# Optimization experiments

Hardware: AMD Instinct MI355X
Metric: run time of the kernel (lower is better)

## Reference

```python
import jax, jax.numpy as jnp
import numpy as np

SCALE = 1.0 / (64 ** 0.5)  # 1/sqrt(dim_key)

def setup_inputs() -> dict:
    key = jax.random.key(0)
    ks = jax.random.split(key, 8)
    B, S, D, H, dk = 4, 2048, 1024, 16, 64
    s = 0.02
    return {
        "values": jax.random.normal(ks[0], (B, S, D), jnp.float32),
        "queries": jax.random.normal(ks[1], (B, S, D), jnp.float32),
        "keys": jax.random.normal(ks[2], (B, S, D), jnp.float32),
        "Wq": jax.random.normal(ks[3], (H, D, dk), jnp.float32) * s,
        "bq": jnp.zeros((H, dk), jnp.float32),
        "Wk": jax.random.normal(ks[4], (H, D, dk), jnp.float32) * s,
        "bk": jnp.zeros((H, dk), jnp.float32),
        "Wv": jax.random.normal(ks[5], (H, D, dk), jnp.float32) * s,
        "bv": jnp.zeros((H, dk), jnp.float32),
        "Wo": jax.random.normal(ks[6], (D, D), jnp.float32) * s,
        "bo": jnp.zeros((D,), jnp.float32),
    }

def reference(values, queries, keys, Wq, bq, Wk, bk, Wv, bv, Wo, bo):
    # Per-head projections, batched across heads: [B,S,D] x [H,D,dk] -> [B,H,S,dk]
    q = jnp.einsum('bsd,hdk->bhsk', queries, Wq) + bq[None, :, None, :]
    k = jnp.einsum('bsd,hdk->bhsk', keys, Wk) + bk[None, :, None, :]
    v = jnp.einsum('bsd,hdk->bhsk', values, Wv) + bv[None, :, None, :]
    # Scaled dot-product scores [B,H,S,S]
    scores = jnp.einsum('bhqk,bhsk->bhqs', q, k) * SCALE
    S = scores.shape[-1]
    causal = jnp.tril(jnp.ones((S, S), bool))
    scores = jnp.where(causal, scores, jnp.float32(-1e19))
    attn = jax.nn.softmax(scores, axis=-1)
    ctx = jnp.einsum('bhqs,bhsk->bhqk', attn, v)  # [B,H,S,dk]
    # Concat heads along last axis (head-major, matching tf.concat order)
    B, H, Sq, dk = ctx.shape
    ctx = jnp.transpose(ctx, (0, 2, 1, 3)).reshape(B, Sq, H * dk)
    return ctx @ Wo + bo
```

## Files before the change

kernel.cpp:

```cpp
#include <hip/hip_runtime.h>
#include <hip/hip_bf16.h>
#include <cstdint>

#define B_ 4
#define H_ 16
#define S_ 2048
#define D_ 1024
#define DK 64
#define QSCALE 0.18033688f

typedef float f32x4 __attribute__((ext_vector_type(4)));
typedef short bf8 __attribute__((ext_vector_type(8)));
typedef unsigned short u16;

__device__ __forceinline__ u16 f2bf(float x){
  union { float f; uint32_t u; } c; c.f = x;
  uint32_t u = c.u;
  uint32_t r = (u + 0x7FFFu + ((u >> 16) & 1u)) >> 16;
  return (u16)r;
}

__device__ __forceinline__ uint32_t pk2bf(float a, float b){
  __hip_bfloat162 t = __float22bfloat162_rn(make_float2(a, b));
  uint32_t r; __builtin_memcpy(&r, &t, 4); return r;
}

__device__ __forceinline__ void gl16(const void* g, void* l){
  __builtin_amdgcn_global_load_lds(
      (const __attribute__((address_space(1))) void*)g,
      (__attribute__((address_space(3))) void*)l, 16, 0, 0);
}

__global__ __launch_bounds__(256) void cvt_in(
    const float* __restrict__ q, const float* __restrict__ k,
    const float* __restrict__ v, u16* __restrict__ o)
{
  const size_t N8 = (size_t)1 << 20;
  const size_t tot = 3 * N8;
  const size_t step = (size_t)gridDim.x * 256;
  for (size_t g0 = (size_t)blockIdx.x*256 + threadIdx.x; g0 < tot; g0 += step){
    int t = (int)(g0 >> 20);
    size_t r = g0 & (N8 - 1);
    const float* src = (t==0 ? q : (t==1 ? k : v));
    const float4* s4 = reinterpret_cast<const float4*>(src + r*8);
    float4 a = s4[0], b = s4[1];
    uint4 w;
    w.x = pk2bf(a.x,a.y); w.y = pk2bf(a.z,a.w);
    w.z = pk2bf(b.x,b.y); w.w = pk2bf(b.z,b.w);
    *reinterpret_cast<uint4*>(o + ((size_t)t << 23) + r*8) = w;
  }
}

__global__ __launch_bounds__(256) void wtrans3(
    const float* __restrict__ Wq, const float* __restrict__ Wk,
    const float* __restrict__ Wv, u16* __restrict__ oq,
    u16* __restrict__ ok, u16* __restrict__ ov)
{
  __shared__ u16 T[64*72];
  const int tid = threadIdx.x;
  const int z = blockIdx.z, t = z >> 4, hh = z & 15;
  const float* src = (t==0 ? Wq : t==1 ? Wk : Wv) + (size_t)hh * (D_*DK);
  u16* dst = (t==0 ? oq : t==1 ? ok : ov) + (size_t)hh * (DK*D_);
  const int r0 = blockIdx.y*64;
  #pragma unroll
  for (int p=0;p<4;++p){
    int r  = p*16 + (tid>>4);
    int c4 = (tid&15)*4;
    float4 v = *reinterpret_cast<const float4*>(&src[(size_t)(r0+r)*DK + c4]);
    uint2 w; w.x = pk2bf(v.x, v.y); w.y = pk2bf(v.z, v.w);
    *reinterpret_cast<uint2*>(&T[r*72 + c4]) = w;
  }
  __syncthreads();
  const int c = tid>>2, rg = (tid&3)*16;
  u16 tmp[16];
  #pragma unroll
  for (int i=0;i<16;++i) tmp[i] = T[(rg+i)*72 + c];
  *reinterpret_cast<bf8*>(&dst[(size_t)c*D_ + r0 + rg])     = *reinterpret_cast<bf8*>(&tmp[0]);
  *reinterpret_cast<bf8*>(&dst[(size_t)c*D_ + r0 + rg + 8]) = *reinterpret_cast<bf8*>(&tmp[8]);
}

__global__ __launch_bounds__(256) void wtrans(
    const float* __restrict__ in, u16* __restrict__ out, int R, int C)
{
  __shared__ u16 T[64*72];
  const int tid = threadIdx.x;
  const int r0 = blockIdx.y*64, c0 = blockIdx.x*64;
  #pragma unroll
  for (int p=0;p<4;++p){
    int r  = p*16 + (tid>>4);
    int c4 = (tid&15)*4;
    float4 v = *reinterpret_cast<const float4*>(&in[(size_t)(r0+r)*C + c0 + c4]);
    uint2 w; w.x = pk2bf(v.x, v.y); w.y = pk2bf(v.z, v.w);
    *reinterpret_cast<uint2*>(&T[r*72 + c4]) = w;
  }
  __syncthreads();
  const int c = tid>>2, rg = (tid&3)*16;
  u16 tmp[16];
  #pragma unroll
  for (int i=0;i<16;++i) tmp[i] = T[(rg+i)*72 + c];
  *reinterpret_cast<bf8*>(&out[(size_t)(c0+c)*R + r0 + rg])     = *reinterpret_cast<bf8*>(&tmp[0]);
  *reinterpret_cast<bf8*>(&out[(size_t)(c0+c)*R + r0 + rg + 8]) = *reinterpret_cast<bf8*>(&tmp[8]);
}

__global__ __launch_bounds__(256) void gemm_qkv(
    const u16* __restrict__ Ab,
    const u16* __restrict__ Bq, const u16* __restrict__ Bk,
    const u16* __restrict__ Bv,
    const float* __restrict__ bq, const float* __restrict__ bk,
    const float* __restrict__ bv,
    u16* __restrict__ oq, u16* __restrict__ ok, u16* __restrict__ ov)
{
  __shared__ u16 As[128*64];
  __shared__ u16 Bs[128*64];
  const int tid = threadIdx.x;
  const int wid = tid>>6, lane = tid&63, g = lane>>4, l15 = lane&15;
  const int z = blockIdx.x >> 9, bid = blockIdx.x & 511;
  const u16* A     = Ab + ((size_t)z << 23);
  const u16*   Bt  = (z==0 ? Bq : z==1 ? Bk : Bv);
  const float* bias= (z==0 ? bq : z==1 ? bk : bv);
  u16* Out         = (z==0 ? oq : z==1 ? ok : ov);
  const float osc  = (z==0 ? QSCALE : 1.0f);
  const int xcd = bid & 7, i = bid >> 3;
  const int cb = i & 7, rb = xcd*8 + (i>>3);
  const int row0 = rb*128, col0 = cb*128;
  const int wr = wid>>1, wc = wid&1;

  f32x4 acc[4][4];
  #pragma unroll
  for (int m=0;m<4;++m)
    #pragma unroll
    for (int n=0;n<4;++n) acc[m][n] = (f32x4){0.f,0.f,0.f,0.f};

  for (int k0 = 0; k0 < D_; k0 += 64) {
    #pragma unroll
    for (int p=0;p<4;++p){
      int r0l = wid*32 + p*8;
      int row = r0l + (lane>>3);
      int ch = (lane&7) ^ (row&7);
      gl16(A  + (size_t)(row0+row)*D_ + k0 + ch*8, &As[r0l*64]);
      gl16(Bt + (size_t)(col0+row)*D_ + k0 + ch*8, &Bs[r0l*64]);
    }
    __syncthreads();

    bf8 af[4][2], bfm[4][2];
    #pragma unroll
    for (int m=0;m<4;++m){
      int row = wr*64 + m*16 + l15;
      af[m][0] = *reinterpret_cast<const bf8*>(&As[row*64 + ((g     ^(row&7))*8)]);
      af[m][1] = *reinterpret_cast<const bf8*>(&As[row*64 + (((4+g) ^(row&7))*8)]);
    }
    #pragma unroll
    for (int n=0;n<4;++n){
      int row = wc*64 + n*16 + l15;
      bfm[n][0] = *reinterpret_cast<const bf8*>(&Bs[row*64 + ((g     ^(row&7))*8)]);
      bfm[n][1] = *reinterpret_cast<const bf8*>(&Bs[row*64 + (((4+g) ^(row&7))*8)]);
    }
    #pragma unroll
    for (int m=0;m<4;++m)
      #pragma unroll
      for (int n=0;n<4;++n){
        acc[m][n] = __builtin_amdgcn_mfma_f32_16x16x32_bf16(af[m][0], bfm[n][0], acc[m][n], 0,0,0);
        acc[m][n] = __builtin_amdgcn_mfma_f32_16x16x32_bf16(af[m][1], bfm[n][1], acc[m][n], 0,0,0);
      }
    __syncthreads();
  }

  #pragma unroll
  for (int m=0;m<4;++m){
    #pragma unroll
    for (int n=0;n<4;++n){
      int col = col0 + wc*64 + n*16 + l15;
      float bs = bias[col];
      if (z == 2){
        int rowb = row0 + wr*64 + m*16 + g*4;
        int b = rowb>>11, s = rowb&2047;
        int h = col>>6, dkk = col&63;
        ushort4 pk;
        pk.x = f2bf(acc[m][n][0]+bs); pk.y = f2bf(acc[m][n][1]+bs);
        pk.z = f2bf(acc[m][n][2]+bs); pk.w = f2bf(acc[m][n][3]+bs);
        *reinterpret_cast<ushort4*>(&Out[(((size_t)(b*H_+h)*DK)+dkk)*S_ + s]) = pk;
      } else {
        #pragma unroll
        for (int r=0;r<4;++r){
          int row = row0 + wr*64 + m*16 + g*4 + r;
          float v = (acc[m][n][r] + bs)*osc;
          int b = row>>11, s = row&2047;
          int h = col>>6, dkk = col&63;
          Out[(((size_t)(b*H_+h)*S_)+s)*DK + dkk] = f2bf(v);
        }
      }
    }
  }
}

__global__ __launch_bounds__(256) void gemm_out(
    const u16* __restrict__ A, const u16* __restrict__ Bt,
    const float* __restrict__ bias, float* __restrict__ Outp)
{
  __shared__ u16 As[128*64];
  __shared__ u16 Bs[128*64];
  const int tid = threadIdx.x;
  const int wid = tid>>6, lane = tid&63, g = lane>>4, l15 = lane&15;
  const int bid = blockIdx.x;
  const int xcd = bid & 7, i = bid >> 3;
  const int cb = i & 7, rb = xcd*8 + (i>>3);
  const int row0 = rb*128, col0 = cb*128;
  const int wr = wid>>1, wc = wid&1;

  f32x4 acc[4][4];
  #pragma unroll
  for (int m=0;m<4;++m)
    #pragma unroll
    for (int n=0;n<4;++n) acc[m][n] = (f32x4){0.f,0.f,0.f,0.f};

  for (int k0 = 0; k0 < D_; k0 += 64) {
    #pragma unroll
    for (int p=0;p<4;++p){
      int r0l = wid*32 + p*8;
      int row = r0l + (lane>>3);
      int ch = (lane&7) ^ (row&7);
      gl16(A  + (size_t)(row0+row)*D_ + k0 + ch*8, &As[r0l*64]);
      gl16(Bt + (size_t)(col0+row)*D_ + k0 + ch*8, &Bs[r0l*64]);
    }
    __syncthreads();

    bf8 af[4][2], bfm[4][2];
    #pragma unroll
    for (int m=0;m<4;++m){
      int row = wr*64 + m*16 + l15;
      af[m][0] = *reinterpret_cast<const bf8*>(&As[row*64 + ((g     ^(row&7))*8)]);
      af[m][1] = *reinterpret_cast<const bf8*>(&As[row*64 + (((4+g) ^(row&7))*8)]);
    }
    #pragma unroll
    for (int n=0;n<4;++n){
      int row = wc*64 + n*16 + l15;
      bfm[n][0] = *reinterpret_cast<const bf8*>(&Bs[row*64 + ((g     ^(row&7))*8)]);
      bfm[n][1] = *reinterpret_cast<const bf8*>(&Bs[row*64 + (((4+g) ^(row&7))*8)]);
    }
    #pragma unroll
    for (int m=0;m<4;++m)
      #pragma unroll
      for (int n=0;n<4;++n){
        acc[m][n] = __builtin_amdgcn_mfma_f32_16x16x32_bf16(af[m][0], bfm[n][0], acc[m][n], 0,0,0);
        acc[m][n] = __builtin_amdgcn_mfma_f32_16x16x32_bf16(af[m][1], bfm[n][1], acc[m][n], 0,0,0);
      }
    __syncthreads();
  }

  #pragma unroll
  for (int m=0;m<4;++m){
    #pragma unroll
    for (int n=0;n<4;++n){
      int col = col0 + wc*64 + n*16 + l15;
      float bs = bias[col];
      #pragma unroll
      for (int r=0;r<4;++r){
        int row = row0 + wr*64 + m*16 + g*4 + r;
        Outp[(size_t)row*D_ + col] = acc[m][n][r] + bs;
      }
    }
  }
}

__global__ __launch_bounds__(256) void attn_kernel(
    const u16* __restrict__ qp, const u16* __restrict__ kp,
    const u16* __restrict__ vt, u16* __restrict__ ctx)
{
  __shared__ u16 Kl[2][64*64];
  __shared__ u16 Vl[2][64*64];
  __shared__ u16 Pl[4][16*72];
  const int tid = threadIdx.x;
  const int wid = tid>>6, lane = tid&63, g = lane>>4, l15 = lane&15;
  const int bid0 = blockIdx.x;
  const int xx = bid0 & 7, yy = bid0 >> 3;
  const int bh = xx + 8*(yy & 7);
  const int j  = yy >> 3;
  const int b = bh >> 4, h = bh & 15;
  const size_t base = (size_t)bh * S_ * DK;

  bf8 ones;
  #pragma unroll
  for (int i=0;i<8;++i) ones[i] = (short)0x3F80;

  const int qts[2] = { j, 31-j };

  #pragma unroll 1
  for (int qi=0; qi<2; ++qi){
    const int qt = qts[qi];
    const int q0 = qt*64;
    const int qrow = q0 + wid*16 + l15;
    bf8 aq0 = *reinterpret_cast<const bf8*>(&qp[base + (size_t)qrow*DK +      g*8]);
    bf8 aq1 = *reinterpret_cast<const bf8*>(&qp[base + (size_t)qrow*DK + 32 + g*8]);

    f32x4 acco[4], acc_l;
    #pragma unroll
    for (int nd=0;nd<4;++nd) acco[nd] = (f32x4){0.f,0.f,0.f,0.f};
    acc_l = (f32x4){0.f,0.f,0.f,0.f};

    auto STAGE = [&](int buf, int kt){
      const int k0 = kt*64;
      #pragma unroll
      for (int p=0;p<2;++p){
        int r0l = wid*16 + p*8;
        int row = r0l + (lane>>3);
        int ch  = (lane&7) ^ (row&7);
        gl16(kp + base + (size_t)(k0+row)*DK + ch*8, &Kl[buf][r0l*64]);
        gl16(vt + base + (size_t)row*S_ + k0 + ch*8, &Vl[buf][r0l*64]);
      }
    };

    int cur = 0;
    STAGE(cur, 0);
    asm volatile("s_waitcnt vmcnt(0)" ::: "memory");
    __syncthreads();

    for (int kt = 0; kt <= qt; ++kt){
      if (kt < qt) STAGE(cur^1, kt+1);

      f32x4 sc[4];
      #pragma unroll
      for (int n=0;n<4;++n){
        int row = n*16 + l15;
        bf8 b0 = *reinterpret_cast<const bf8*>(&Kl[cur][row*64 + ((g     ^(row&7))*8)]);
        bf8 b1 = *reinterpret_cast<const bf8*>(&Kl[cur][row*64 + (((4+g) ^(row&7))*8)]);
        f32x4 z = (f32x4){0.f,0.f,0.f,0.f};
        z = __builtin_amdgcn_mfma_f32_16x16x32_bf16(aq0, b0, z, 0,0,0);
        z = __builtin_amdgcn_mfma_f32_16x16x32_bf16(aq1, b1, z, 0,0,0);
        sc[n] = z;
      }
      if (kt == qt){
        #pragma unroll
        for (int n=0;n<4;++n){
          #pragma unroll
          for (int r=0;r<4;++r){
            int qg = wid*16 + g*4 + r;
            int kg = n*16 + l15;
            if (kg > qg) sc[n][r] = -1e30f;
          }
        }
      }
      #pragma unroll
      for (int n=0;n<4;++n){
        #pragma unroll
        for (int r=0;r<4;++r){
          float p = __builtin_amdgcn_exp2f(sc[n][r]);
          union { float f; uint32_t u; } cu; cu.f = p;
          Pl[wid][(g*4 + r)*72 + n*16 + l15] = (u16)(cu.u >> 16);
        }
      }
      asm volatile("s_waitcnt lgkmcnt(0)" ::: "memory");
      __builtin_amdgcn_sched_barrier(0);

      bf8 pa0 = *reinterpret_cast<const bf8*>(&Pl[wid][l15*72 +      g*8]);
      bf8 pa1 = *reinterpret_cast<const bf8*>(&Pl[wid][l15*72 + 32 + g*8]);
      acc_l = __builtin_amdgcn_mfma_f32_16x16x32_bf16(pa0, ones, acc_l, 0,0,0);
      acc_l = __builtin_amdgcn_mfma_f32_16x16x32_bf16(pa1, ones, acc_l, 0,0,0);
      #pragma unroll
      for (int nd=0;nd<4;++nd){
        int row = nd*16 + l15;
        bf8 v0 = *reinterpret_cast<const bf8*>(&Vl[cur][row*64 + ((g     ^(row&7))*8)]);
        bf8 v1 = *reinterpret_cast<const bf8*>(&Vl[cur][row*64 + (((4+g) ^(row&7))*8)]);
        acco[nd] = __builtin_amdgcn_mfma_f32_16x16x32_bf16(pa0, v0, acco[nd], 0,0,0);
        acco[nd] = __builtin_amdgcn_mfma_f32_16x16x32_bf16(pa1, v1, acco[nd], 0,0,0);
      }
      asm volatile("s_waitcnt vmcnt(0)" ::: "memory");
      __syncthreads();
      cur ^= 1;
    }

    float rl[4];
    #pragma unroll
    for (int r=0;r<4;++r) rl[r] = __builtin_amdgcn_rcpf(acc_l[r]);
    #pragma unroll
    for (int nd=0;nd<4;++nd){
      #pragma unroll
      for (int r=0;r<4;++r){
        int qg = q0 + wid*16 + g*4 + r;
        float v = acco[nd][r] * rl[r];
        ctx[((size_t)(b*S_) + qg)*D_ + h*DK + nd*16 + l15] = f2bf(v);
      }
    }
  }
}

extern "C" void kernel_launch(void* const* d_in, const int* in_sizes, int n_in,
                              void* d_out, int out_size, void* d_ws, size_t ws_size,
                              hipStream_t stream)
{
  const float* values  = (const float*)d_in[0];
  const float* queries = (const float*)d_in[1];
  const float* keys    = (const float*)d_in[2];
  const float* Wq = (const float*)d_in[3];
  const float* bq = (const float*)d_in[4];
  const float* Wk = (const float*)d_in[5];
  const float* bk = (const float*)d_in[6];
  const float* Wv = (const float*)d_in[7];
  const float* bv = (const float*)d_in[8];
  const float* Wo = (const float*)d_in[9];
  const float* bo = (const float*)d_in[10];
  float* out = (float*)d_out;

  const size_t NE = (size_t)B_*H_*S_*DK;
  const size_t WE = (size_t)D_*D_;
  u16* cvt = (u16*)d_ws;
  u16* qp  = cvt + 3*NE;
  u16* kp  = qp + NE;
  u16* vtb = kp + NE;
  u16* wtq = vtb + NE;
  u16* wtk = wtq + WE;
  u16* wtv = wtk + WE;
  u16* wto = wtv + WE;
  u16* ctx = cvt;

  cvt_in<<<3072, 256, 0, stream>>>(queries, keys, values, cvt);
  wtrans3<<<dim3(1,16,48), 256, 0, stream>>>(Wq, Wk, Wv, wtq, wtk, wtv);
  wtrans<<<dim3(16,16,1), 256, 0, stream>>>(Wo, wto, D_, D_);
  gemm_qkv<<<1536, 256, 0, stream>>>(cvt, wtq, wtk, wtv,
                                     bq, bk, bv, qp, kp, vtb);
  attn_kernel<<<1024, 256, 0, stream>>>(qp, kp, vtb, ctx);
  gemm_out<<<512, 256, 0, stream>>>(ctx, wto, bo, out);
}
```

Baseline: 199.5 us.

## Double query tile per block to 128 rows for K/V reuse in attention

The attention kernel now processes 128 query rows per block (32 per wave, two 16-row subtiles) instead of 64, so each staged K/V tile feeds twice as many MFMAs. The grid is halved to 512 blocks, with the paired causal tiles remapped to j and 15-j. This cuts K/V global and LDS staging traffic and barrier count per unit of work. In exchange it doubles accumulator registers, which may lower occupancy, and leaves fewer blocks to fill the GPU.

Result: faster. 190.1 us (-4.7%).

```diff
diff --git a/kernel.cpp b/kernel.cpp
--- a/kernel.cpp
+++ b/kernel.cpp
@@ -268,13 +268,13 @@
 {
   __shared__ u16 Kl[2][64*64];
   __shared__ u16 Vl[2][64*64];
-  __shared__ u16 Pl[4][16*72];
+  __shared__ u16 Pl[4][32*72];
   const int tid = threadIdx.x;
   const int wid = tid>>6, lane = tid&63, g = lane>>4, l15 = lane&15;
   const int bid0 = blockIdx.x;
   const int xx = bid0 & 7, yy = bid0 >> 3;
-  const int bh = xx + 8*(yy & 7);
-  const int j  = yy >> 3;
+  const int bh = xx + 8*(yy >> 3);
+  const int jj = yy & 7;
   const int b = bh >> 4, h = bh & 15;
   const size_t base = (size_t)bh * S_ * DK;
 
@@ -282,20 +282,27 @@
   #pragma unroll
   for (int i=0;i<8;++i) ones[i] = (short)0x3F80;
 
-  const int qts[2] = { j, 31-j };
+  const int qts[2] = { jj, 15-jj };
 
   #pragma unroll 1
   for (int qi=0; qi<2; ++qi){
     const int qt = qts[qi];
-    const int q0 = qt*64;
-    const int qrow = q0 + wid*16 + l15;
-    bf8 aq0 = *reinterpret_cast<const bf8*>(&qp[base + (size_t)qrow*DK +      g*8]);
-    bf8 aq1 = *reinterpret_cast<const bf8*>(&qp[base + (size_t)qrow*DK + 32 + g*8]);
-
-    f32x4 acco[4], acc_l;
-    #pragma unroll
-    for (int nd=0;nd<4;++nd) acco[nd] = (f32x4){0.f,0.f,0.f,0.f};
-    acc_l = (f32x4){0.f,0.f,0.f,0.f};
+    const int Q0 = qt*128;
+    bf8 aq[2][2];
+    #pragma unroll
+    for (int qs=0;qs<2;++qs){
+      int qrow = Q0 + wid*32 + qs*16 + l15;
+      aq[qs][0] = *reinterpret_cast<const bf8*>(&qp[base + (size_t)qrow*DK +      g*8]);
+      aq[qs][1] = *reinterpret_cast<const bf8*>(&qp[base + (size_t)qrow*DK + 32 + g*8]);
+    }
+
+    f32x4 acco[2][4], acc_l[2];
+    #pragma unroll
+    for (int qs=0;qs<2;++qs){
+      #pragma unroll
+      for (int nd=0;nd<4;++nd) acco[qs][nd] = (f32x4){0.f,0.f,0.f,0.f};
+      acc_l[qs] = (f32x4){0.f,0.f,0.f,0.f};
+    }
 
     auto STAGE = [&](int buf, int kt){
       const int k0 = kt*64;
@@ -309,75 +316,96 @@
       }
     };
 
+    const int nk = 2*qt + 2;
     int cur = 0;
     STAGE(cur, 0);
     asm volatile("s_waitcnt vmcnt(0)" ::: "memory");
     __syncthreads();
 
-    for (int kt = 0; kt <= qt; ++kt){
-      if (kt < qt) STAGE(cur^1, kt+1);
-
-      f32x4 sc[4];
+    for (int kt = 0; kt < nk; ++kt){
+      if (kt < nk-1) STAGE(cur^1, kt+1);
+
+      f32x4 sc[2][4];
       #pragma unroll
       for (int n=0;n<4;++n){
         int row = n*16 + l15;
         bf8 b0 = *reinterpret_cast<const bf8*>(&Kl[cur][row*64 + ((g     ^(row&7))*8)]);
         bf8 b1 = *reinterpret_cast<const bf8*>(&Kl[cur][row*64 + (((4+g) ^(row&7))*8)]);
-        f32x4 z = (f32x4){0.f,0.f,0.f,0.f};
-        z = __builtin_amdgcn_mfma_f32_16x16x32_bf16(aq0, b0, z, 0,0,0);
-        z = __builtin_amdgcn_mfma_f32_16x16x32_bf16(aq1, b1, z, 0,0,0);
-        sc[n] = z;
-      }
-      if (kt == qt){
+        #pragma unroll
+        for (int qs=0;qs<2;++qs){
+          f32x4 z = (f32x4){0.f,0.f,0.f,0.f};
+          z = __builtin_amdgcn_mfma_f32_16x16x32_bf16(aq[qs][0], b0, z, 0,0,0);
+          z = __builtin_amdgcn_mfma_f32_16x16x32_bf16(aq[qs][1], b1, z, 0,0,0);
+          sc[qs][n] = z;
+        }
+      }
+      if (kt >= nk-2){
+        const int k0 = kt*64;
+        #pragma unroll
+        for (int qs=0;qs<2;++qs){
+          #pragma unroll
+          for (int n=0;n<4;++n){
+            #pragma unroll
+            for (int r=0;r<4;++r){
+              int qg = Q0 + wid*32 + qs*16 + g*4 + r;
+              int kg = k0 + n*16 + l15;
+              if (kg > qg) sc[qs][n][r] = -1e30f;
+            }
+          }
+        }
+      }
+      #pragma unroll
+      for (int qs=0;qs<2;++qs){
         #pragma unroll
         for (int n=0;n<4;++n){
           #pragma unroll
           for (int r=0;r<4;++r){
-            int qg = wid*16 + g*4 + r;
-            int kg = n*16 + l15;
-            if (kg > qg) sc[n][r] = -1e30f;
+            float p = __builtin_amdgcn_exp2f(sc[qs][n][r]);
+            union { float f; uint32_t u; } cu; cu.f = p;
+            Pl[wid][(qs*16 + g*4 + r)*72 + n*16 + l15] = (u16)(cu.u >> 16);
           }
-        }
-      }
-      #pragma unroll
-      for (int n=0;n<4;++n){
-        #pragma unroll
-        for (int r=0;r<4;++r){
-          float p = __builtin_amdgcn_exp2f(sc[n][r]);
-          union { float f; uint32_t u; } cu; cu.f = p;
-          Pl[wid][(g*4 + r)*72 + n*16 + l15] = (u16)(cu.u >> 16);
         }
       }
       asm volatile("s_waitcnt lgkmcnt(0)" ::: "memory");
       __builtin_amdgcn_sched_barrier(0);
 
-      bf8 pa0 = *reinterpret_cast<const bf8*>(&Pl[wid][l15*72 +      g*8]);
-      bf8 pa1 = *reinterpret_cast<const bf8*>(&Pl[wid][l15*72 + 32 + g*8]);
-      acc_l = __builtin_amdgcn_mfma_f32_16x16x32_bf16(pa0, ones, acc_l, 0,0,0);
-      acc_l = __builtin_amdgcn_mfma_f32_16x16x32_bf16(pa1, ones, acc_l, 0,0,0);
+      bf8 pa[2][2];
+      #pragma unroll
+      for (int qs=0;qs<2;++qs){
+        pa[qs][0] = *reinterpret_cast<const bf8*>(&Pl[wid][(qs*16 + l15)*72 +      g*8]);
+        pa[qs][1] = *reinterpret_cast<const bf8*>(&Pl[wid][(qs*16 + l15)*72 + 32 + g*8]);
+        acc_l[qs] = __builtin_amdgcn_mfma_f32_16x16x32_bf16(pa[qs][0], ones, acc_l[qs], 0,0,0);
+        acc_l[qs] = __builtin_amdgcn_mfma_f32_16x16x32_bf16(pa[qs][1], ones, acc_l[qs], 0,0,0);
+      }
       #pragma unroll
       for (int nd=0;nd<4;++nd){
         int row = nd*16 + l15;
         bf8 v0 = *reinterpret_cast<const bf8*>(&Vl[cur][row*64 + ((g     ^(row&7))*8)]);
         bf8 v1 = *reinterpret_cast<const bf8*>(&Vl[cur][row*64 + (((4+g) ^(row&7))*8)]);
-        acco[nd] = __builtin_amdgcn_mfma_f32_16x16x32_bf16(pa0, v0, acco[nd], 0,0,0);
-        acco[nd] = __builtin_amdgcn_mfma_f32_16x16x32_bf16(pa1, v1, acco[nd], 0,0,0);
+        #pragma unroll
+        for (int qs=0;qs<2;++qs){
+          acco[qs][nd] = __builtin_amdgcn_mfma_f32_16x16x32_bf16(pa[qs][0], v0, acco[qs][nd], 0,0,0);
+          acco[qs][nd] = __builtin_amdgcn_mfma_f32_16x16x32_bf16(pa[qs][1], v1, acco[qs][nd], 0,0,0);
+        }
       }
       asm volatile("s_waitcnt vmcnt(0)" ::: "memory");
       __syncthreads();
       cur ^= 1;
     }
 
-    float rl[4];
-    #pragma unroll
-    for (int r=0;r<4;++r) rl[r] = __builtin_amdgcn_rcpf(acc_l[r]);
-    #pragma unroll
-    for (int nd=0;nd<4;++nd){
-      #pragma unroll
-      for (int r=0;r<4;++r){
-        int qg = q0 + wid*16 + g*4 + r;
-        float v = acco[nd][r] * rl[r];
-        ctx[((size_t)(b*S_) + qg)*D_ + h*DK + nd*16 + l15] = f2bf(v);
+    #pragma unroll
+    for (int qs=0;qs<2;++qs){
+      float rl[4];
+      #pragma unroll
+      for (int r=0;r<4;++r) rl[r] = __builtin_amdgcn_rcpf(acc_l[qs][r]);
+      #pragma unroll
+      for (int nd=0;nd<4;++nd){
+        #pragma unroll
+        for (int r=0;r<4;++r){
+          int qg = Q0 + wid*32 + qs*16 + g*4 + r;
+          float v = acco[qs][nd][r] * rl[r];
+          ctx[((size_t)(b*S_) + qg)*D_ + h*DK + nd*16 + l15] = f2bf(v);
+        }
       }
     }
   }
@@ -417,6 +445,6 @@
   wtrans<<<dim3(16,16,1), 256, 0, stream>>>(Wo, wto, D_, D_);
   gemm_qkv<<<1536, 256, 0, stream>>>(cvt, wtq, wtk, wtv,
                                      bq, bk, bv, qp, kp, vtb);
-  attn_kernel<<<1024, 256, 0, stream>>>(qp, kp, vtb, ctx);
+  attn_kernel<<<512, 256, 0, stream>>>(qp, kp, vtb, ctx);
   gemm_out<<<512, 256, 0, stream>>>(ctx, wto, bo, out);
 }
```
